# Kernel tuning notes

Hardware: AMD Instinct MI355X
Metric: run time of the kernel (lower is better)

Reference implementation:

```python
import jax, jax.numpy as jnp
import numpy as np

THETA = 10000.0
NUM_HEADS = 16


def _rope(x, positions):
    # x: [B, H, S, Dk] (fp32), positions: [B, S] int
    d_k = x.shape[-1]
    k = jnp.arange(0, d_k, 2, dtype=jnp.float32)
    freqs = THETA ** (-k / d_k)                      # [Dk/2]
    angles = positions[..., None].astype(jnp.float32) * freqs  # [B, S, Dk/2]
    cos = jnp.cos(angles)[:, None, :, :]             # [B, 1, S, Dk/2]
    sin = jnp.sin(angles)[:, None, :, :]
    xr = x.reshape(*x.shape[:-1], d_k // 2, 2)
    x_even, x_odd = xr[..., 0], xr[..., 1]
    rot_even = x_even * cos - x_odd * sin
    rot_odd = x_even * sin + x_odd * cos
    out = jnp.stack([rot_even, rot_odd], axis=-1)
    return out.reshape(x.shape)


def setup_inputs() -> dict:
    key = jax.random.key(0)
    ks = jax.random.split(key, 6)
    B, S, D = 2, 2048, 1024
    std = (2.0 / (D + D)) ** 0.5
    x = jax.random.normal(ks[0], (B, S, D), dtype=jnp.float32)
    Wq = jax.random.normal(ks[1], (D, D), dtype=jnp.float32) * std
    Wk = jax.random.normal(ks[2], (D, D), dtype=jnp.float32) * std
    Wv = jax.random.normal(ks[3], (D, D), dtype=jnp.float32) * std
    Wo = jax.random.normal(ks[4], (D, D), dtype=jnp.float32) * std
    token_positions = jnp.broadcast_to(jnp.arange(S, dtype=jnp.int32), (B, S))
    return {"x": x, "Wq": Wq, "Wk": Wk, "Wv": Wv, "Wo": Wo,
            "token_positions": token_positions}


def reference(x, Wq, Wk, Wv, Wo, token_positions):
    B, S, D = x.shape
    H = NUM_HEADS
    Dk = D // H
    # QKV projections (no bias): y = x @ W.T
    def proj(W):
        return (x @ W.T).reshape(B, S, H, Dk).transpose(0, 2, 1, 3)  # [B,H,S,Dk]
    Q, K, V = proj(Wq), proj(Wk), proj(Wv)
    Q = _rope(Q, token_positions)
    K = _rope(K, token_positions)
    scale = 1.0 / jnp.sqrt(jnp.float32(Dk))
    scores = jnp.einsum('bhqd,bhkd->bhqk', Q, K) * scale  # [B,H,S,S]
    causal = jnp.tril(jnp.ones((S, S), dtype=bool))
    scores = jnp.where(causal, scores, -jnp.inf)
    attn = jax.nn.softmax(scores.astype(jnp.float32), axis=-1)
    out = jnp.einsum('bhqk,bhkd->bhqd', attn, V)          # [B,H,S,Dk]
    out = out.transpose(0, 2, 1, 3).reshape(B, S, D)
    return out @ Wo.T
```

## Files before the change

kernel.cpp:

```cpp
#include <hip/hip_runtime.h>
#include <math.h>

#define D_MODEL 1024
#define NHEADS 16
#define DK 64
#define SEQ 2048
#define BATCH 2
#define MROWS (BATCH * SEQ)

typedef __attribute__((ext_vector_type(8))) short bfrag8;
typedef __attribute__((ext_vector_type(4))) float f32x4;
typedef unsigned short u16;
typedef __attribute__((ext_vector_type(8))) u16 u16x8;
typedef __attribute__((ext_vector_type(4))) u16 u16x4;

#define GLOBAL_AS(p) ((const __attribute__((address_space(1))) void*)(p))
#define LDS_AS(p)    ((__attribute__((address_space(3))) void*)(p))

__device__ inline u16 f2bf(float f) {
  union { float f; unsigned u; } c; c.f = f;
  unsigned r = c.u + 0x7FFF + ((c.u >> 16) & 1);
  return (u16)(r >> 16);
}

__device__ inline unsigned pack_bf2(float lo, float hi) {
  return __builtin_amdgcn_perm(__float_as_uint(hi), __float_as_uint(lo), 0x07060302);
}

__global__ __launch_bounds__(256)
void build_rope_tab(const int* __restrict__ pos, float2* __restrict__ tab) {
  int idx = blockIdx.x * 256 + threadIdx.x;
  int i = idx & 31, bs = idx >> 5;
  float p = (float)pos[bs];
  float freq = expf(-(float)i * 0.2878231366242558f);
  float sn, cs;
  sincosf(p * freq, &sn, &cs);
  tab[idx] = make_float2(cs, sn);
}

struct CvtPtrs { const float* src[5]; };

__global__ __launch_bounds__(256)
void convert_inputs(CvtPtrs p, u16* __restrict__ dst) {
  size_t base = ((size_t)blockIdx.x * 256 + threadIdx.x) * 4;
  const size_t XSZ = (size_t)MROWS * D_MODEL;
  const float* s; size_t off;
  if (base < XSZ) { s = p.src[0]; off = base; }
  else {
    size_t j = base - XSZ;
    s = p.src[1 + (int)(j >> 20)];
    off = j & ((1u << 20) - 1);
  }
  float4 v = *(const float4*)(s + off);
  u16 o[4] = { f2bf(v.x), f2bf(v.y), f2bf(v.z), f2bf(v.w) };
  *(u16x4*)(dst + base) = *(u16x4*)o;
}

__device__ inline void gemm_core(const u16* __restrict__ A, const u16* __restrict__ B,
                                 int m0, int n0, u16* As, u16* Bs,
                                 f32x4 acc[4][4]) {
  const int tid = threadIdx.x;
  const int w = tid >> 6, lane = tid & 63;
  const int l15 = lane & 15, quad = lane >> 4;
  const int wm = w >> 1, wn = w & 1;
  const int srow = tid >> 2;
  const int scol = (tid & 3) * 8;

  #pragma unroll
  for (int mi = 0; mi < 4; ++mi)
    #pragma unroll
    for (int ni = 0; ni < 4; ++ni) acc[mi][ni] = (f32x4)0.f;

  for (int k0 = 0; k0 < D_MODEL; k0 += 32) {
    __syncthreads();
    #pragma unroll
    for (int i = 0; i < 2; ++i) {
      const u16* ga = A + (size_t)((i * 64 + srow) + m0) * D_MODEL + k0 + scol;
      const u16* gb = B + (size_t)((i * 64 + srow) + n0) * D_MODEL + k0 + scol;
      __builtin_amdgcn_global_load_lds(GLOBAL_AS(ga), LDS_AS(&As[(i * 64 + w * 16) * 32]), 16, 0, 0);
      __builtin_amdgcn_global_load_lds(GLOBAL_AS(gb), LDS_AS(&Bs[(i * 64 + w * 16) * 32]), 16, 0, 0);
    }
    __syncthreads();

    bfrag8 af[4], bfr[4];
    #pragma unroll
    for (int i = 0; i < 4; ++i) {
      af[i]  = *(const bfrag8*)&As[(wm * 64 + i * 16 + l15) * 32 + quad * 8];
      bfr[i] = *(const bfrag8*)&Bs[(wn * 64 + i * 16 + l15) * 32 + quad * 8];
    }
    #pragma unroll
    for (int mi = 0; mi < 4; ++mi)
      #pragma unroll
      for (int ni = 0; ni < 4; ++ni)
        acc[mi][ni] = __builtin_amdgcn_mfma_f32_16x16x32_bf16(af[mi], bfr[ni], acc[mi][ni], 0, 0, 0);
  }
}

struct QKVArgs { const u16* A[3]; const u16* B[3]; u16* dst[3]; const float2* tab; };

__global__ __launch_bounds__(256)
void gemm_qkv_fused(QKVArgs p) {
  __shared__ u16 As[128 * 32];
  __shared__ u16 Bs[128 * 32];
  const int z = blockIdx.z;
  const int bi = blockIdx.x;
  int m0, n0;
  if (z < 2) { m0 = (bi & 7) * 128; n0 = (bi >> 3) * 128; }
  else       { m0 = (bi >> 3) * 128; n0 = (bi & 7) * 128; }
  f32x4 acc[4][4];
  gemm_core(p.A[z], p.B[z], m0, n0, As, Bs, acc);

  const int tid = threadIdx.x;
  const int w = tid >> 6, lane = tid & 63;
  const int l15 = lane & 15, quad = lane >> 4;
  const int wm = w >> 1, wn = w & 1;
  u16* dst = p.dst[z];

  if (z < 2) {
    const int head = (m0 + wm * 64) >> 6;
    const float scale = (z == 0) ? 0.125f : 1.0f;
    #pragma unroll
    for (int ni = 0; ni < 4; ++ni) {
      int sg = n0 + wn * 64 + ni * 16 + l15;
      int b = sg >> 11;
      int s = sg & (SEQ - 1);
      size_t ho = ((size_t)(b * NHEADS + head)) * SEQ * DK;
      #pragma unroll
      for (int mi = 0; mi < 4; ++mi) {
        float4 t = *(const float4*)&p.tab[(size_t)sg * 32 + mi * 8 + quad * 2];
        float e0 = acc[mi][ni][0], o0 = acc[mi][ni][1];
        float e1 = acc[mi][ni][2], o1 = acc[mi][ni][3];
        u16x4 ov = { f2bf((e0 * t.x - o0 * t.y) * scale),
                     f2bf((e0 * t.y + o0 * t.x) * scale),
                     f2bf((e1 * t.z - o1 * t.w) * scale),
                     f2bf((e1 * t.w + o1 * t.z) * scale) };
        *(u16x4*)&dst[ho + (size_t)s * DK + mi * 16 + quad * 4] = ov;
      }
    }
  } else {
    const int b = m0 >> 11;
    const int head = (n0 >> 6) + wn;
    const size_t ho = ((size_t)(b * NHEADS + head)) * SEQ * DK;
    const int row_base = m0 + wm * 64;
    #pragma unroll
    for (int mi = 0; mi < 4; ++mi)
      #pragma unroll
      for (int ni = 0; ni < 4; ++ni) {
        int d = ni * 16 + l15;
        int sb = (row_base + mi * 16 + quad * 4) & (SEQ - 1);
        u16 o[4];
        #pragma unroll
        for (int r = 0; r < 4; ++r) o[r] = f2bf(acc[mi][ni][r]);
        *(u16x4*)&dst[ho + (size_t)d * SEQ + sb] = *(u16x4*)o;
      }
  }
}

__global__ __launch_bounds__(256)
void gemm_out_bf16(const u16* __restrict__ A, const u16* __restrict__ B,
                   float* __restrict__ C) {
  __shared__ u16 As[128 * 32];
  __shared__ u16 Bs[128 * 32];
  const int m0 = blockIdx.y * 128, n0 = blockIdx.x * 128;
  f32x4 acc[4][4];
  gemm_core(A, B, m0, n0, As, Bs, acc);

  const int tid = threadIdx.x;
  const int w = tid >> 6, lane = tid & 63;
  const int l15 = lane & 15, quad = lane >> 4;
  const int wm = w >> 1, wn = w & 1;
  #pragma unroll
  for (int mi = 0; mi < 4; ++mi)
    #pragma unroll
    for (int ni = 0; ni < 4; ++ni)
      #pragma unroll
      for (int r = 0; r < 4; ++r) {
        int row = m0 + wm * 64 + mi * 16 + quad * 4 + r;
        int col = n0 + wn * 64 + ni * 16 + l15;
        C[(size_t)row * D_MODEL + col] = acc[mi][ni][r];
      }
}

#define PSTR 72

__global__ __launch_bounds__(256)
void attn_mfma(const u16* __restrict__ Qbf, const u16* __restrict__ Kbf,
               const u16* __restrict__ Vtb, u16* __restrict__ obb) {
  __shared__ u16 Ks[64 * 64];
  __shared__ u16 Vt[64 * 64];
  __shared__ u16 Ps[4][16 * PSTR];

  const int tid = threadIdx.x;
  const int w = tid >> 6, lane = tid & 63;
  const int l15 = lane & 15, quad = lane >> 4;
  const int h = blockIdx.y, b = blockIdx.z;
  const int qt = ((h ^ b) & 1) ? (31 - blockIdx.x) : blockIdx.x;
  const int q0 = qt * 64;
  const size_t ho = ((size_t)(b * NHEADS + h)) * SEQ * DK;
  const int qrow_base = q0 + w * 16;

  bfrag8 qf[2];
  #pragma unroll
  for (int hh = 0; hh < 2; ++hh)
    qf[hh] = *(const bfrag8*)&Qbf[ho + (size_t)(qrow_base + l15) * DK + hh * 32 + quad * 8];

  f32x4 oacc[4];
  float m_ = -1e30f, l_ = 0.f;
  #pragma unroll
  for (int n0 = 0; n0 < 4; ++n0) oacc[n0] = (f32x4)0.f;

  const int ntiles = qt + 1;
  for (int t = 0; t < ntiles; ++t) {
    const int j0 = t * 64;
    __syncthreads();
    #pragma unroll
    for (int i = 0; i < 2; ++i) {
      int row = i * 32 + w * 8 + (lane >> 3);
      int c = (lane & 7) ^ (row & 7);
      const u16* ksrc = Kbf + ho + (size_t)(j0 + row) * DK + c * 8;
      const u16* vsrc = Vtb + ho + (size_t)row * SEQ + j0 + c * 8;
      __builtin_amdgcn_global_load_lds(GLOBAL_AS(ksrc), LDS_AS(&Ks[(i * 4 + w) * 512]), 16, 0, 0);
      __builtin_amdgcn_global_load_lds(GLOBAL_AS(vsrc), LDS_AS(&Vt[(i * 4 + w) * 512]), 16, 0, 0);
    }
    __syncthreads();

    f32x4 sc[4];
    #pragma unroll
    for (int st = 0; st < 4; ++st) {
      int key = st * 16 + l15;
      int sw = l15 & 7;
      bfrag8 kf0 = *(const bfrag8*)&Ks[key * 64 + ((quad ^ sw) * 8)];
      bfrag8 kf1 = *(const bfrag8*)&Ks[key * 64 + (((4 + quad) ^ sw) * 8)];
      sc[st] = __builtin_amdgcn_mfma_f32_16x16x32_bf16(kf0, qf[0], (f32x4)0.f, 0, 0, 0);
      sc[st] = __builtin_amdgcn_mfma_f32_16x16x32_bf16(kf1, qf[1], sc[st], 0, 0, 0);
    }

    if (j0 + 63 > qrow_base) {
      #pragma unroll
      for (int st = 0; st < 4; ++st)
        #pragma unroll
        for (int r = 0; r < 4; ++r) {
          int key = j0 + st * 16 + quad * 4 + r;
          if (key > qrow_base + l15) sc[st][r] = -1e30f;
        }
    }

    float mx = sc[0][0];
    #pragma unroll
    for (int st = 0; st < 4; ++st)
      #pragma unroll
      for (int r = 0; r < 4; ++r) mx = fmaxf(mx, sc[st][r]);
    mx = fmaxf(mx, __shfl_xor(mx, 16));
    mx = fmaxf(mx, __shfl_xor(mx, 32));
    float mnew = fmaxf(m_, mx);
    float alpha = __expf(m_ - mnew);
    m_ = mnew;
    float pv[4][4], rs = 0.f;
    #pragma unroll
    for (int st = 0; st < 4; ++st)
      #pragma unroll
      for (int r = 0; r < 4; ++r) { pv[st][r] = __expf(sc[st][r] - mnew); rs += pv[st][r]; }
    rs += __shfl_xor(rs, 16);
    rs += __shfl_xor(rs, 32);
    l_ = l_ * alpha + rs;
    #pragma unroll
    for (int n0 = 0; n0 < 4; ++n0) oacc[n0] *= alpha;

    #pragma unroll
    for (int st = 0; st < 4; ++st) {
      uint2 pk = { pack_bf2(pv[st][0], pv[st][1]), pack_bf2(pv[st][2], pv[st][3]) };
      *(uint2*)&Ps[w][l15 * PSTR + st * 16 + quad * 4] = pk;
    }
    __asm__ volatile("s_waitcnt lgkmcnt(0)" ::: "memory");

    bfrag8 pf[2];
    #pragma unroll
    for (int kc = 0; kc < 2; ++kc)
      pf[kc] = *(const bfrag8*)&Ps[w][l15 * PSTR + kc * 32 + quad * 8];
    #pragma unroll
    for (int n0 = 0; n0 < 4; ++n0) {
      int sw = l15 & 7;
      #pragma unroll
      for (int kc = 0; kc < 2; ++kc) {
        bfrag8 vf = *(const bfrag8*)&Vt[(n0 * 16 + l15) * 64 + (((kc * 4 + quad) ^ sw) * 8)];
        oacc[n0] = __builtin_amdgcn_mfma_f32_16x16x32_bf16(vf, pf[kc], oacc[n0], 0, 0, 0);
      }
    }
  }

  float inv = 1.f / l_;
  int q = qrow_base + l15;
  #pragma unroll
  for (int n0 = 0; n0 < 4; ++n0) {
    u16x4 ov = { f2bf(oacc[n0][0] * inv), f2bf(oacc[n0][1] * inv),
                 f2bf(oacc[n0][2] * inv), f2bf(oacc[n0][3] * inv) };
    *(u16x4*)&obb[(size_t)(b * SEQ + q) * D_MODEL + h * DK + n0 * 16 + quad * 4] = ov;
  }
}

extern "C" void kernel_launch(void* const* d_in, const int* in_sizes, int n_in,
                              void* d_out, int out_size, void* d_ws, size_t ws_size,
                              hipStream_t stream) {
  const float* x  = (const float*)d_in[0];
  const float* Wq = (const float*)d_in[1];
  const float* Wk = (const float*)d_in[2];
  const float* Wv = (const float*)d_in[3];
  const float* Wo = (const float*)d_in[4];
  const int* pos  = (const int*)d_in[5];

  const size_t XSZ = (size_t)MROWS * D_MODEL;
  const size_t WSZ = (size_t)D_MODEL * D_MODEL;

  u16* bfb = (u16*)d_ws;
  u16* xb  = bfb;
  u16* wqb = xb  + XSZ;
  u16* wkb = wqb + WSZ;
  u16* wvb = wkb + WSZ;
  u16* wob = wvb + WSZ;
  u16* Qbf = wob + WSZ;
  u16* Kbf = Qbf + XSZ;
  u16* Vtb = Kbf + XSZ;
  u16* obb = Vtb + XSZ;
  float2* tab = (float2*)(obb + XSZ);

  build_rope_tab<<<(BATCH * SEQ * 32) / 256, 256, 0, stream>>>(pos, tab);

  CvtPtrs cp; cp.src[0] = x; cp.src[1] = Wq; cp.src[2] = Wk; cp.src[3] = Wv; cp.src[4] = Wo;
  size_t cvtElems = XSZ + 4 * WSZ;
  convert_inputs<<<(int)(cvtElems / 4 / 256), 256, 0, stream>>>(cp, xb);

  QKVArgs qp;
  qp.A[0] = wqb; qp.A[1] = wkb; qp.A[2] = xb;
  qp.B[0] = xb;  qp.B[1] = xb;  qp.B[2] = wvb;
  qp.dst[0] = Qbf; qp.dst[1] = Kbf; qp.dst[2] = Vtb;
  qp.tab = tab;
  gemm_qkv_fused<<<dim3(256, 1, 3), 256, 0, stream>>>(qp);

  attn_mfma<<<dim3(SEQ / 64, NHEADS, BATCH), 256, 0, stream>>>(Qbf, Kbf, Vtb, obb);

  gemm_out_bf16<<<dim3(D_MODEL / 128, MROWS / 128), 256, 0, stream>>>(obb, wob, (float*)d_out);
}
```

Measured before the change: 200.3 us.

## Double-buffer attention K/V tiles, use exp2 softmax, reshape output GEMM tiles

The attention kernel now double-buffers K and V tiles in LDS. It prefetches the next tile with async global-to-LDS loads and waits on vmcnt with raw barriers, so memory latency overlaps compute. Softmax switches to exp2, with log2(e) folded into the Q scale in the QKV epilogue. Block order is linearised so paired long and short causal tiles are adjacent. The output GEMM moves to 128x64 tiles with an inline K-loop to launch more blocks, at the cost of less reuse per block.

New measurement: 229.9 us. +14.8%, slower.

```diff
diff --git a/kernel.cpp b/kernel.cpp
--- a/kernel.cpp
+++ b/kernel.cpp
@@ -16,6 +16,10 @@
 
 #define GLOBAL_AS(p) ((const __attribute__((address_space(1))) void*)(p))
 #define LDS_AS(p)    ((__attribute__((address_space(3))) void*)(p))
+
+#define RAW_BARRIER()  __asm__ volatile("s_barrier" ::: "memory")
+#define WAIT_VM4()     __asm__ volatile("s_waitcnt vmcnt(4)" ::: "memory")
+#define WAIT_VM0()     __asm__ volatile("s_waitcnt vmcnt(0)" ::: "memory")
 
 __device__ inline u16 f2bf(float f) {
   union { float f; unsigned u; } c; c.f = f;
@@ -118,7 +122,7 @@
 
   if (z < 2) {
     const int head = (m0 + wm * 64) >> 6;
-    const float scale = (z == 0) ? 0.125f : 1.0f;
+    const float scale = (z == 0) ? 0.125f * 1.4426950408889634f : 1.0f;
     #pragma unroll
     for (int ni = 0; ni < 4; ++ni) {
       int sg = n0 + wn * 64 + ni * 16 + l15;
@@ -160,23 +164,58 @@
 void gemm_out_bf16(const u16* __restrict__ A, const u16* __restrict__ B,
                    float* __restrict__ C) {
   __shared__ u16 As[128 * 32];
-  __shared__ u16 Bs[128 * 32];
-  const int m0 = blockIdx.y * 128, n0 = blockIdx.x * 128;
-  f32x4 acc[4][4];
-  gemm_core(A, B, m0, n0, As, Bs, acc);
-
+  __shared__ u16 Bs[64 * 32];
+  const int m0 = blockIdx.y * 128, n0 = blockIdx.x * 64;
   const int tid = threadIdx.x;
   const int w = tid >> 6, lane = tid & 63;
   const int l15 = lane & 15, quad = lane >> 4;
   const int wm = w >> 1, wn = w & 1;
+  const int lrow = lane >> 2;
+  const int lcol = (lane & 3) * 8;
+
+  f32x4 acc[4][2];
   #pragma unroll
   for (int mi = 0; mi < 4; ++mi)
     #pragma unroll
-    for (int ni = 0; ni < 4; ++ni)
+    for (int ni = 0; ni < 2; ++ni) acc[mi][ni] = (f32x4)0.f;
+
+  for (int k0 = 0; k0 < D_MODEL; k0 += 32) {
+    __syncthreads();
+    #pragma unroll
+    for (int i = 0; i < 2; ++i) {
+      int row = (i * 4 + w) * 16 + lrow;
+      const u16* ga = A + (size_t)(m0 + row) * D_MODEL + k0 + lcol;
+      __builtin_amdgcn_global_load_lds(GLOBAL_AS(ga), LDS_AS(&As[(i * 4 + w) * 16 * 32]), 16, 0, 0);
+    }
+    {
+      int row = w * 16 + lrow;
+      const u16* gb = B + (size_t)(n0 + row) * D_MODEL + k0 + lcol;
+      __builtin_amdgcn_global_load_lds(GLOBAL_AS(gb), LDS_AS(&Bs[w * 16 * 32]), 16, 0, 0);
+    }
+    __syncthreads();
+
+    bfrag8 af[4], bfr[2];
+    #pragma unroll
+    for (int i = 0; i < 4; ++i)
+      af[i] = *(const bfrag8*)&As[(wm * 64 + i * 16 + l15) * 32 + quad * 8];
+    #pragma unroll
+    for (int i = 0; i < 2; ++i)
+      bfr[i] = *(const bfrag8*)&Bs[(wn * 32 + i * 16 + l15) * 32 + quad * 8];
+    #pragma unroll
+    for (int mi = 0; mi < 4; ++mi)
+      #pragma unroll
+      for (int ni = 0; ni < 2; ++ni)
+        acc[mi][ni] = __builtin_amdgcn_mfma_f32_16x16x32_bf16(af[mi], bfr[ni], acc[mi][ni], 0, 0, 0);
+  }
+
+  #pragma unroll
+  for (int mi = 0; mi < 4; ++mi)
+    #pragma unroll
+    for (int ni = 0; ni < 2; ++ni)
       #pragma unroll
       for (int r = 0; r < 4; ++r) {
         int row = m0 + wm * 64 + mi * 16 + quad * 4 + r;
-        int col = n0 + wn * 64 + ni * 16 + l15;
+        int col = n0 + wn * 32 + ni * 16 + l15;
         C[(size_t)row * D_MODEL + col] = acc[mi][ni][r];
       }
 }
@@ -186,18 +225,21 @@
 __global__ __launch_bounds__(256)
 void attn_mfma(const u16* __restrict__ Qbf, const u16* __restrict__ Kbf,
                const u16* __restrict__ Vtb, u16* __restrict__ obb) {
-  __shared__ u16 Ks[64 * 64];
-  __shared__ u16 Vt[64 * 64];
+  __shared__ u16 Ks[2][64 * 64];
+  __shared__ u16 Vt[2][64 * 64];
   __shared__ u16 Ps[4][16 * PSTR];
 
   const int tid = threadIdx.x;
   const int w = tid >> 6, lane = tid & 63;
   const int l15 = lane & 15, quad = lane >> 4;
-  const int h = blockIdx.y, b = blockIdx.z;
-  const int qt = ((h ^ b) & 1) ? (31 - blockIdx.x) : blockIdx.x;
-  const int q0 = qt * 64;
-  const size_t ho = ((size_t)(b * NHEADS + h)) * SEQ * DK;
-  const int qrow_base = q0 + w * 16;
+  const int lin = blockIdx.x;
+  const int u = lin >> 1, par = lin & 1;
+  const int hb = u >> 4;
+  const int qh = u & 15;
+  const int qt = par ? (31 - qh) : qh;
+  const int b = hb >> 4, h = hb & 15;
+  const size_t ho = (size_t)hb * SEQ * DK;
+  const int qrow_base = qt * 64 + w * 16;
 
   bfrag8 qf[2];
   #pragma unroll
@@ -209,28 +251,45 @@
   #pragma unroll
   for (int n0 = 0; n0 < 4; ++n0) oacc[n0] = (f32x4)0.f;
 
+  const int srow0 = w * 8 + (lane >> 3);
+  const int sc0 = ((lane & 7) ^ (srow0 & 7)) * 8;
+  const int srow1 = 32 + srow0;
+  const int sc1 = ((lane & 7) ^ (srow1 & 7)) * 8;
+
+  #define STAGE(T, BUF) do {                                                       \
+    int j0_ = (T) * 64;                                                            \
+    __builtin_amdgcn_global_load_lds(GLOBAL_AS(Kbf + ho + (size_t)(j0_ + srow0) * DK + sc0), \
+                                     LDS_AS(&Ks[BUF][(0 * 4 + w) * 512]), 16, 0, 0); \
+    __builtin_amdgcn_global_load_lds(GLOBAL_AS(Vtb + ho + (size_t)srow0 * SEQ + j0_ + sc0), \
+                                     LDS_AS(&Vt[BUF][(0 * 4 + w) * 512]), 16, 0, 0); \
+    __builtin_amdgcn_global_load_lds(GLOBAL_AS(Kbf + ho + (size_t)(j0_ + srow1) * DK + sc1), \
+                                     LDS_AS(&Ks[BUF][(1 * 4 + w) * 512]), 16, 0, 0); \
+    __builtin_amdgcn_global_load_lds(GLOBAL_AS(Vtb + ho + (size_t)srow1 * SEQ + j0_ + sc1), \
+                                     LDS_AS(&Vt[BUF][(1 * 4 + w) * 512]), 16, 0, 0); \
+  } while (0)
+
   const int ntiles = qt + 1;
+  STAGE(0, 0);
+
   for (int t = 0; t < ntiles; ++t) {
     const int j0 = t * 64;
-    __syncthreads();
-    #pragma unroll
-    for (int i = 0; i < 2; ++i) {
-      int row = i * 32 + w * 8 + (lane >> 3);
-      int c = (lane & 7) ^ (row & 7);
-      const u16* ksrc = Kbf + ho + (size_t)(j0 + row) * DK + c * 8;
-      const u16* vsrc = Vtb + ho + (size_t)row * SEQ + j0 + c * 8;
-      __builtin_amdgcn_global_load_lds(GLOBAL_AS(ksrc), LDS_AS(&Ks[(i * 4 + w) * 512]), 16, 0, 0);
-      __builtin_amdgcn_global_load_lds(GLOBAL_AS(vsrc), LDS_AS(&Vt[(i * 4 + w) * 512]), 16, 0, 0);
-    }
-    __syncthreads();
+    const int buf = t & 1;
+    RAW_BARRIER();
+    if (t + 1 < ntiles) {
+      STAGE(t + 1, buf ^ 1);
+      WAIT_VM4();
+    } else {
+      WAIT_VM0();
+    }
+    RAW_BARRIER();
 
     f32x4 sc[4];
     #pragma unroll
     for (int st = 0; st < 4; ++st) {
       int key = st * 16 + l15;
       int sw = l15 & 7;
-      bfrag8 kf0 = *(const bfrag8*)&Ks[key * 64 + ((quad ^ sw) * 8)];
-      bfrag8 kf1 = *(const bfrag8*)&Ks[key * 64 + (((4 + quad) ^ sw) * 8)];
+      bfrag8 kf0 = *(const bfrag8*)&Ks[buf][key * 64 + ((quad ^ sw) * 8)];
+      bfrag8 kf1 = *(const bfrag8*)&Ks[buf][key * 64 + (((4 + quad) ^ sw) * 8)];
       sc[st] = __builtin_amdgcn_mfma_f32_16x16x32_bf16(kf0, qf[0], (f32x4)0.f, 0, 0, 0);
       sc[st] = __builtin_amdgcn_mfma_f32_16x16x32_bf16(kf1, qf[1], sc[st], 0, 0, 0);
     }
@@ -253,13 +312,16 @@
     mx = fmaxf(mx, __shfl_xor(mx, 16));
     mx = fmaxf(mx, __shfl_xor(mx, 32));
     float mnew = fmaxf(m_, mx);
-    float alpha = __expf(m_ - mnew);
+    float alpha = __builtin_amdgcn_exp2f(m_ - mnew);
     m_ = mnew;
     float pv[4][4], rs = 0.f;
     #pragma unroll
     for (int st = 0; st < 4; ++st)
       #pragma unroll
-      for (int r = 0; r < 4; ++r) { pv[st][r] = __expf(sc[st][r] - mnew); rs += pv[st][r]; }
+      for (int r = 0; r < 4; ++r) {
+        pv[st][r] = __builtin_amdgcn_exp2f(sc[st][r] - mnew);
+        rs += pv[st][r];
+      }
     rs += __shfl_xor(rs, 16);
     rs += __shfl_xor(rs, 32);
     l_ = l_ * alpha + rs;
@@ -282,11 +344,12 @@
       int sw = l15 & 7;
       #pragma unroll
       for (int kc = 0; kc < 2; ++kc) {
-        bfrag8 vf = *(const bfrag8*)&Vt[(n0 * 16 + l15) * 64 + (((kc * 4 + quad) ^ sw) * 8)];
+        bfrag8 vf = *(const bfrag8*)&Vt[buf][(n0 * 16 + l15) * 64 + (((kc * 4 + quad) ^ sw) * 8)];
         oacc[n0] = __builtin_amdgcn_mfma_f32_16x16x32_bf16(vf, pf[kc], oacc[n0], 0, 0, 0);
       }
     }
   }
+  #undef STAGE
 
   float inv = 1.f / l_;
   int q = qrow_base + l15;
@@ -336,7 +399,7 @@
   qp.tab = tab;
   gemm_qkv_fused<<<dim3(256, 1, 3), 256, 0, stream>>>(qp);
 
-  attn_mfma<<<dim3(SEQ / 64, NHEADS, BATCH), 256, 0, stream>>>(Qbf, Kbf, Vtb, obb);
-
-  gemm_out_bf16<<<dim3(D_MODEL / 128, MROWS / 128), 256, 0, stream>>>(obb, wob, (float*)d_out);
-}
+  attn_mfma<<<dim3(1024), 256, 0, stream>>>(Qbf, Kbf, Vtb, obb);
+
+  gemm_out_bf16<<<dim3(D_MODEL / 64, MROWS / 128), 256, 0, stream>>>(obb, wob, (float*)d_out);
+}
```
